# Kernel tuning notes

Measured on AMD Instinct MI355X. Metric: run time of the kernel, lower is better.

The kernel has to match this reference:

```python
import jax, jax.numpy as jnp
import numpy as np

B, N, K, H = 8, 1024, 16, 4
EMB = 1024

def lrelu(x):
    return jnp.where(x >= 0, x, 0.2 * x)

def bn(x, g, b):
    # eval-mode BatchNorm with running_mean=0, running_var=1
    inv = 1.0 / np.sqrt(1.0 + 1e-5)
    shape = (1, -1) + (1,) * (x.ndim - 2)
    return x * (g * inv).reshape(shape) + b.reshape(shape)

def conv1x1(x, w):
    # 1x1 conv == channel matmul; x: (B,C,...), w: (O,C)
    return jnp.einsum('bc...,oc->bo...', x, w)

def knn_idx(x, k):
    # x: (B,C,N); negative squared pairwise distance, top-k largest = nearest
    inner = -2.0 * jnp.einsum('bcn,bcm->bnm', x, x)
    xx = jnp.sum(x * x, axis=1)                      # (B,N)
    pd = -xx[:, :, None] - inner - xx[:, None, :]
    return jax.lax.top_k(pd, k)[1]                   # (B,N,k)

def graph_feature(x, idx):
    b = x.shape[0]
    xt = jnp.transpose(x, (0, 2, 1))                 # (B,N,C)
    nbr = xt[jnp.arange(b)[:, None, None], idx]      # (B,N,K,C) gather
    ctr = jnp.broadcast_to(xt[:, :, None, :], nbr.shape)
    f = jnp.concatenate([nbr - ctr, ctr], axis=-1)   # (B,N,K,2C)
    return jnp.transpose(f, (0, 3, 1, 2))            # (B,2C,N,K)

def mak(x, y, w0, g0, b0, wm, gm, bm, w1, go, bo, ws, gs, bs, out_ch, in_ch):
    # Multi-head adaptive kernel: generate per-point (out,in,H) weights from y, apply to x
    Bc, _, Nc, Kc = x.shape
    y = lrelu(bn(conv1x1(y, w0), g0, b0))
    y = lrelu(bn(conv1x1(y, wm), gm, bm))
    y = conv1x1(y, w1)                               # (B, out*in*H, N, K)
    w = jnp.transpose(y, (0, 2, 3, 1)).reshape(Bc, Nc, Kc, out_ch, in_ch, H)
    xt = jnp.transpose(x, (0, 2, 3, 1))              # (B,N,K,in)
    # per-head matmul then sum over heads == single einsum over i and h
    out = jnp.einsum('bnkoih,bnki->bonk', w, xt)
    out = bn(out, go, bo)
    idt = bn(conv1x1(x, ws), gs, bs)                 # shortcut (in != out)
    return lrelu(out + idt)


def setup_inputs() -> dict:
    ks = jax.random.split(jax.random.key(0), 48)
    it = iter(range(48))
    def nrm(shape, fan):
        return jax.random.normal(ks[next(it)], shape, jnp.float32) / np.sqrt(fan)
    def gam(c):
        return jax.random.uniform(ks[next(it)], (c,), jnp.float32, 0.5, 1.5)
    def bet(c):
        return 0.1 * jax.random.normal(ks[next(it)], (c,), jnp.float32)
    d = {}
    d['x'] = jax.random.normal(ks[next(it)], (B, 3, N), jnp.float32)
    def mak_params(p, feat_c):
        d[p + '_w0'] = nrm((64, feat_c), feat_c); d[p + '_g0'] = gam(64); d[p + '_b0'] = bet(64)
        d[p + '_wm'] = nrm((64, 64), 64); d[p + '_gm'] = gam(64); d[p + '_bm'] = bet(64)
        d[p + '_w1'] = nrm((64 * 6 * H, 64), 64)
        d[p + '_go'] = gam(64); d[p + '_bo'] = bet(64)
        d[p + '_ws'] = nrm((64, 6), 6); d[p + '_gs'] = gam(64); d[p + '_bs'] = bet(64)
    mak_params('m1', 6)
    mak_params('m2', 128)
    d['w3'] = nrm((128, 128), 128); d['g3'] = gam(128); d['b3'] = bet(128)
    d['w4'] = nrm((256, 256), 256); d['g4'] = gam(256); d['b4'] = bet(256)
    d['w5'] = nrm((EMB, 512), 512); d['g5'] = gam(EMB); d['b5'] = bet(EMB)
    d['wl1'] = nrm((512, 2 * EMB), 2 * EMB); d['bn4_g'] = gam(512); d['bn4_b'] = bet(512)
    d['wl2'] = nrm((256, 512), 512); d['bl2'] = bet(256); d['bn5_g'] = gam(256); d['bn5_b'] = bet(256)
    d['wl3'] = nrm((49, 256), 256); d['bl3'] = bet(49)
    return d


def reference(x, m1_w0, m1_g0, m1_b0, m1_wm, m1_gm, m1_bm, m1_w1, m1_go, m1_bo, m1_ws, m1_gs, m1_bs, m2_w0, m2_g0, m2_b0, m2_wm, m2_gm, m2_bm, m2_w1, m2_go, m2_bo, m2_ws, m2_gs, m2_bs, w3, g3, b3, w4, g4, b4, w5, g5, b5, wl1, bn4_g, bn4_b, wl2, bl2, bn5_g, bn5_b, wl3, bl3):
    idx = knn_idx(x, K)                              # common_idx from points
    geo = graph_feature(x, idx)                      # (B,6,N,K); feat_x == geo_x at stage 1
    h = mak(geo, geo, m1_w0, m1_g0, m1_b0, m1_wm, m1_gm, m1_bm, m1_w1, m1_go, m1_bo, m1_ws, m1_gs, m1_bs, 64, 6)
    x1 = h.max(axis=-1)                              # (B,64,N)
    feat2 = graph_feature(x1, idx)                   # (B,128,N,K)
    h = mak(geo, feat2, m2_w0, m2_g0, m2_b0, m2_wm, m2_gm, m2_bm, m2_w1, m2_go, m2_bo, m2_ws, m2_gs, m2_bs, 64, 6)
    x2 = h.max(axis=-1)                              # (B,64,N)
    x3 = lrelu(bn(conv1x1(graph_feature(x2, idx), w3), g3, b3)).max(axis=-1)   # (B,128,N)
    x4 = lrelu(bn(conv1x1(graph_feature(x3, idx), w4), g4, b4)).max(axis=-1)   # (B,256,N)
    xc = jnp.concatenate([x1, x2, x3, x4], axis=1)   # (B,512,N)
    x5 = lrelu(bn(conv1x1(xc, w5), g5, b5))          # (B,EMB,N)
    xp = jnp.concatenate([x5.max(axis=-1), x5.mean(axis=-1)], axis=1)  # (B,2*EMB)
    xf = lrelu(bn(xp @ wl1.T, bn4_g, bn4_b))
    xf = lrelu(bn(xf @ wl2.T + bl2, bn5_g, bn5_b))
    return xf @ wl3.T + bl3                           # (B,49)
```

## Files before the change

kernel.cpp:

```cpp
#include <hip/hip_runtime.h>
#include <math.h>

#define BB 8
#define NN 1024
#define KK 16
#define NKP (NN*KK)
#define BN_INV 0.99999500003749981f

typedef unsigned short u16;
typedef __attribute__((ext_vector_type(8))) short short8;
typedef __attribute__((ext_vector_type(4))) float f32x4;

#define MFMA16(a,b,c) __builtin_amdgcn_mfma_f32_16x16x32_bf16(a,b,c,0,0,0)

__device__ __forceinline__ float lrelu(float v) { return v >= 0.f ? v : 0.2f * v; }

__device__ __forceinline__ u16 f2bf(float f) {
  union { float f; unsigned u; } v; v.f = f;
  unsigned r = v.u + 0x7fff + ((v.u >> 16) & 1);
  return (u16)(r >> 16);
}
__device__ __forceinline__ float bf2f(u16 s) {
  union { unsigned u; float f; } v; v.u = ((unsigned)s) << 16;
  return v.f;
}

constexpr size_t OFF_IDX   = 0;
constexpr size_t OFF_X1P   = 524288;
constexpr size_t OFF_X2P   = 1572864;
constexpr size_t OFF_X3P   = 2621440;
constexpr size_t OFF_MUV   = 2621440;
constexpr size_t OFF_X4P   = 4718592;
constexpr size_t OFF_GEO   = 4718592;
constexpr size_t OFF_PMAX  = 8912896;
constexpr size_t OFF_PSUM  = 9437184;
constexpr size_t OFF_XP    = 9961472;
constexpr size_t OFF_XF1   = 10027008;
constexpr size_t OFF_XF2   = 10043392;
constexpr size_t OFF_M1WM  = 10055680;
constexpr size_t OFF_M1W1S = 10063872;
constexpr size_t OFF_M2W0S = 10117120;
constexpr size_t OFF_M2WM  = 10133504;
constexpr size_t OFF_M2W1S = 10141696;
constexpr size_t OFF_W3S   = 10194944;
constexpr size_t OFF_W4S   = 10227712;
constexpr size_t OFF_W5    = 10358784;
constexpr size_t OFF_WL1T  = 11407360;
constexpr size_t OFF_WL2T  = 15601664;
constexpr size_t OFF_WL3T  = 16125952;
constexpr size_t OFF_UV3   = 16177152;
constexpr size_t OFF_EY0   = 16177152;
constexpr size_t OFF_UV4   = 20371456;

struct SSeg { const float* w; const float* g; u16* dst; int O; int C; int cpl2; int ch; int stk; int start; };
struct SArgs { SSeg seg[6]; int total; };

__global__ __launch_bounds__(256) void prep_scale_bf16(SArgs a) {
  const int tid = blockIdx.x * 256 + threadIdx.x;
  if (tid >= a.total) return;
  int s = 0;
  #pragma unroll
  for (int i = 1; i < 6; ++i) if (tid >= a.seg[i].start) s = i;
  const SSeg sg = a.seg[s];
  const int e = tid - sg.start;
  const int o2 = e >> sg.cpl2;
  const int c = e & ((1 << sg.cpl2) - 1);
  float v = 0.f;
  if (sg.stk) {
    const int half = sg.O >> 1;
    const int o = o2 & (half - 1);
    const int CIN = 2 * sg.C;
    const float wd = sg.w[o * CIN + c];
    v = (o2 < half) ? wd : (sg.w[o * CIN + sg.C + c] - wd);
    v *= sg.g[o] * BN_INV;
  } else if (c < sg.C) {
    v = sg.w[o2 * sg.C + c];
    if (sg.ch && c >= sg.ch) v -= sg.w[o2 * sg.C + c - sg.ch];
    v *= sg.g[o2] * BN_INV;
  }
  sg.dst[(size_t)(c >> 5) * (sg.O * 32) + o2 * 32 + (c & 31)] = f2bf(v);
}

__global__ __launch_bounds__(256) void prep_w1s_bf16(
    const float* __restrict__ w1a, const float* __restrict__ wsa,
    const float* __restrict__ goa, const float* __restrict__ gsa,
    const float* __restrict__ w1b, const float* __restrict__ wsb,
    const float* __restrict__ gob, const float* __restrict__ gsb,
    u16* __restrict__ dsta, u16* __restrict__ dstb) {
  const int tid = blockIdx.x * 256 + threadIdx.x;
  if (tid >= 64 * 416) return;
  const float* w1 = blockIdx.y ? w1b : w1a;
  const float* wsm = blockIdx.y ? wsb : wsa;
  const float* go = blockIdx.y ? gob : goa;
  const float* gs = blockIdx.y ? gsb : gsa;
  u16* dst = blockIdx.y ? dstb : dsta;
  const int o = tid / 416, ci = tid - o * 416;
  float v = 0.f;
  if (ci < 384) {
    const int ii = ci >> 6, ch = ci & 63;
    const int base = (o * 24 + ii * 4) * 64 + ch;
    v = go[o] * BN_INV * (w1[base] + w1[base + 64] + w1[base + 128] + w1[base + 192]);
  } else if (ci < 390) {
    v = gs[o] * BN_INV * wsm[o * 6 + (ci - 384)];
  }
  dst[(size_t)(ci >> 5) * 2048 + o * 32 + (ci & 31)] = f2bf(v);
}

struct TSeg { const float* w; const float* g; float* dst; int O; int C; int start; };
struct TArgs3 { TSeg seg[3]; int total; };

__global__ __launch_bounds__(256) void prep_transpose_f32(TArgs3 a) {
  const int tid = blockIdx.x * 256 + threadIdx.x;
  if (tid >= a.total) return;
  int s = 0;
  #pragma unroll
  for (int i = 1; i < 3; ++i) if (tid >= a.seg[i].start) s = i;
  const TSeg sg = a.seg[s];
  const int e = tid - sg.start;
  const int c = e / sg.O;
  const int o = e - c * sg.O;
  float v = sg.w[o * sg.C + c];
  if (sg.g) v *= sg.g[o] * BN_INV;
  sg.dst[e] = v;
}

__global__ __launch_bounds__(256) void knn_kernel(const float* __restrict__ x, int* __restrict__ idxout) {
  const int wid  = (blockIdx.x * blockDim.x + threadIdx.x) >> 6;
  const int lane = threadIdx.x & 63;
  const int b = wid >> 10;
  const int n = wid & (NN - 1);
  const float* xb = x + b * 3 * NN;
  const float x0n = xb[n], x1n = xb[NN + n], x2n = xb[2 * NN + n];
  const float xxn = x0n * x0n + x1n * x1n + x2n * x2n;
  float pd[16];
  #pragma unroll
  for (int j = 0; j < 16; ++j) {
    const int m = j * 64 + lane;
    const float x0 = xb[m], x1 = xb[NN + m], x2 = xb[2 * NN + m];
    const float dot = x0n * x0 + x1n * x1 + x2n * x2;
    const float xxm = x0 * x0 + x1 * x1 + x2 * x2;
    pd[j] = 2.f * dot - xxn - xxm;
  }
  for (int r = 0; r < 16; ++r) {
    float bv = pd[0]; int bj = 0;
    #pragma unroll
    for (int j = 1; j < 16; ++j) if (pd[j] > bv) { bv = pd[j]; bj = j; }
    int bm = bj * 64 + lane;
    #pragma unroll
    for (int off = 32; off > 0; off >>= 1) {
      const float ov = __shfl_down(bv, off);
      const int   om = __shfl_down(bm, off);
      if (ov > bv || (ov == bv && om < bm)) { bv = ov; bm = om; }
    }
    bm = __shfl(bm, 0);
    if (lane == 0) idxout[wid * KK + r] = bm;
    const int  cj   = bm >> 6;
    const bool mine = (bm & 63) == lane;
    #pragma unroll
    for (int j = 0; j < 16; ++j) if (mine && j == cj) pd[j] = -INFINITY;
  }
}

__device__ __forceinline__ short8 bfrag64(const u16* T, int pl, int quad, int c0) {
  const int pos = ((c0 >> 3) + quad) ^ (pl & 7);
  return *(const short8*)(T + pl * 64 + pos * 8);
}
__device__ __forceinline__ void writeD64(u16* T, int pl, int quad, const f32x4 a,
                                         const float* __restrict__ bias, int obase) {
  union { ushort4 v; u16 s[4]; } pk;
  #pragma unroll
  for (int r = 0; r < 4; ++r) pk.s[r] = f2bf(lrelu(a[r] + bias[obase + quad * 4 + r]));
  const int g = (obase + quad * 4) >> 3;
  const int pos = g ^ (pl & 7);
  *(ushort4*)(T + pl * 64 + pos * 8 + (quad & 1) * 4) = pk.v;
}

__global__ __launch_bounds__(256) void mak1_uv(
    const float* __restrict__ x, const float* __restrict__ w0,
    const float* __restrict__ g0, const float* __restrict__ b0,
    u16* __restrict__ MUV) {
  const int tid = blockIdx.x * 256 + threadIdx.x;
  if (tid >= BB * NN * 64) return;
  const int o = tid & 63;
  const int p = tid >> 6;
  const int b = p >> 10, n = p & (NN - 1);
  const float* xb = x + b * 3 * NN;
  const float gg = g0[o] * BN_INV;
  float u = 0.f, v = 0.f;
  #pragma unroll
  for (int i = 0; i < 3; ++i) {
    const float wd = w0[o * 6 + i];
    const float wc = w0[o * 6 + 3 + i];
    const float c = xb[i * NN + n];
    u += wd * c;
    v += (wc - wd) * c;
  }
  MUV[(size_t)p * 128 + o]      = f2bf(gg * u);
  MUV[(size_t)p * 128 + 64 + o] = f2bf(gg * v + b0[o]);
}

__global__ __launch_bounds__(256) void mak_edge_build(
    const float* __restrict__ x, const int* __restrict__ idxb,
    const u16* __restrict__ MUV, u16* __restrict__ EY0,
    u16* __restrict__ GEO, int writeGeo) {
  const int tid = blockIdx.x * 256 + threadIdx.x;
  const int cg = tid & 7;
  const int e = tid >> 3;
  const int b = e >> 14;
  const int nk = e & 16383;
  const int n = nk >> 4;
  const int nbr = idxb[e] & (NN - 1);
  union { uint4 q; u16 s[8]; } uu, vv, rr;
  uu.q = *(const uint4*)(MUV + (size_t)(b * NN + nbr) * 128 + cg * 8);
  vv.q = *(const uint4*)(MUV + (size_t)(b * NN + n) * 128 + 64 + cg * 8);
  #pragma unroll
  for (int j = 0; j < 8; ++j) rr.s[j] = f2bf(lrelu(bf2f(uu.s[j]) + bf2f(vv.s[j])));
  *(uint4*)(EY0 + (size_t)e * 64 + cg * 8) = rr.q;
  if (writeGeo && cg == 0) {
    const float* xb = x + b * 3 * NN;
    union { uint4 q; u16 s[8]; } g;
    #pragma unroll
    for (int i = 0; i < 3; ++i) {
      const float fc = xb[i * NN + n];
      g.s[i]     = f2bf(xb[i * NN + nbr] - fc);
      g.s[3 + i] = f2bf(fc);
    }
    g.s[6] = 0; g.s[7] = 0;
    *(uint4*)(GEO + (size_t)e * 8) = g.q;
  }
}

__global__ __launch_bounds__(256) void mak23_mfma(
    const u16* __restrict__ EY0, const u16* __restrict__ GEO,
    const u16* __restrict__ wmb, const float* __restrict__ bmv,
    const u16* __restrict__ w1s, const float* __restrict__ bov, const float* __restrict__ bsv,
    u16* __restrict__ Xoutp) {
  __shared__ __align__(16) u16 YMs[64 * 64];

  const int t = threadIdx.x;
  const int b = blockIdx.z;
  const int w = t >> 6, l = t & 63;
  const int quad = l >> 4, l15 = l & 15;
  const int pl = w * 16 + l15;
  const int cq8 = quad * 8;
  const int nvtx = blockIdx.x * 4 + w;
  const size_t eL = ((size_t)(b * NN + nvtx)) * 16 + l15;

  union { short8 v; u16 s[8]; } gq;
  gq.v = *(const short8*)(GEO + eL * 8);
  float ge[6];
  #pragma unroll
  for (int ii = 0; ii < 6; ++ii) ge[ii] = bf2f(gq.s[ii]);
  const short8 bgv = (quad == 0) ? gq.v : (short8)(short)0;

  f32x4 acc[4];
  #pragma unroll
  for (int i = 0; i < 4; ++i) acc[i] = (f32x4)0.f;
  #pragma unroll
  for (int kc = 0; kc < 2; ++kc) {
    const short8 bf = *(const short8*)(EY0 + eL * 64 + kc * 32 + cq8);
    #pragma unroll
    for (int at = 0; at < 4; ++at) {
      const short8 af = *(const short8*)(wmb + (size_t)(kc * 64 + at * 16 + l15) * 32 + cq8);
      acc[at] = MFMA16(af, bf, acc[at]);
    }
  }
  #pragma unroll
  for (int at = 0; at < 4; ++at) writeD64(YMs, pl, quad, acc[at], bmv, at * 16);

  short8 bf3[2];
  #pragma unroll
  for (int kc = 0; kc < 2; ++kc) bf3[kc] = bfrag64(YMs, pl, quad, kc * 32);

  #pragma unroll
  for (int i = 0; i < 4; ++i) acc[i] = (f32x4)0.f;
  #pragma unroll
  for (int ii = 0; ii < 6; ++ii) {
    f32x4 tacc[4];
    #pragma unroll
    for (int i = 0; i < 4; ++i) tacc[i] = (f32x4)0.f;
    #pragma unroll
    for (int kc = 0; kc < 2; ++kc) {
      #pragma unroll
      for (int at = 0; at < 4; ++at) {
        const short8 af = *(const short8*)(w1s + (size_t)((ii * 2 + kc) * 64 + at * 16 + l15) * 32 + cq8);
        tacc[at] = MFMA16(af, bf3[kc], tacc[at]);
      }
    }
    const float g = ge[ii];
    #pragma unroll
    for (int at = 0; at < 4; ++at) acc[at] += g * tacc[at];
  }
  #pragma unroll
  for (int at = 0; at < 4; ++at) {
    const short8 af = *(const short8*)(w1s + (size_t)(12 * 64 + at * 16 + l15) * 32 + cq8);
    acc[at] = MFMA16(af, bgv, acc[at]);
  }

  u16* orow = Xoutp + (size_t)(b * NN + nvtx) * 64;
  #pragma unroll
  for (int at = 0; at < 4; ++at) {
    union { ushort4 v; u16 s[4]; } pk;
    #pragma unroll
    for (int r = 0; r < 4; ++r) {
      const int o = at * 16 + quad * 4 + r;
      float v = lrelu(acc[at][r] + bov[o] + bsv[o]);
      v = fmaxf(v, __shfl_xor(v, 1));
      v = fmaxf(v, __shfl_xor(v, 2));
      v = fmaxf(v, __shfl_xor(v, 4));
      v = fmaxf(v, __shfl_xor(v, 8));
      pk.s[r] = f2bf(v);
    }
    if (l15 == 0) *(ushort4*)(orow + at * 16 + quad * 4) = pk.v;
  }
}

template<int CH, int COUT2>
__global__ __launch_bounds__(256) void dense_uv(
    const u16* __restrict__ srcp, const u16* __restrict__ w2,
    const float* __restrict__ bias, u16* __restrict__ UV) {
  constexpr int COUT = COUT2 / 2;
  constexpr int NCH = CH / 32;
  const int t = threadIdx.x;
  const int b = blockIdx.z;
  const int w = t >> 6, l = t & 63;
  const int quad = l >> 4, l15 = l & 15;
  const int cq8 = quad * 8;
  int n0, ow0;
  if constexpr (COUT2 >= 256) { n0 = blockIdx.x * 64; ow0 = blockIdx.y * 256 + w * 64; }
  else { n0 = blockIdx.x * 128 + (w >> 1) * 64; ow0 = (w & 1) * 64; }

  f32x4 acc[4][4];
  #pragma unroll
  for (int i = 0; i < 4; ++i)
    #pragma unroll
    for (int j = 0; j < 4; ++j) acc[i][j] = (f32x4)0.f;

  #pragma unroll
  for (int k = 0; k < NCH; ++k) {
    short8 bfr[4];
    #pragma unroll
    for (int pg = 0; pg < 4; ++pg) {
      const int n = n0 + pg * 16 + l15;
      bfr[pg] = *(const short8*)(srcp + (size_t)(b * NN + n) * CH + k * 32 + cq8);
    }
    #pragma unroll
    for (int at = 0; at < 4; ++at) {
      const short8 af = *(const short8*)(w2 + ((size_t)(k * COUT2 + ow0 + at * 16 + l15)) * 32 + cq8);
      #pragma unroll
      for (int pg = 0; pg < 4; ++pg) acc[at][pg] = MFMA16(af, bfr[pg], acc[at][pg]);
    }
  }

  #pragma unroll
  for (int at = 0; at < 4; ++at) {
    const int o0 = ow0 + at * 16 + quad * 4;
    const bool isv = (o0 >= COUT);
    float bb[4];
    #pragma unroll
    for (int r = 0; r < 4; ++r) bb[r] = isv ? bias[o0 + r - COUT] : 0.f;
    #pragma unroll
    for (int pg = 0; pg < 4; ++pg) {
      const int n = n0 + pg * 16 + l15;
      union { ushort4 v; u16 s[4]; } pk;
      #pragma unroll
      for (int r = 0; r < 4; ++r) pk.s[r] = f2bf(acc[at][pg][r] + bb[r]);
      *(ushort4*)(UV + (size_t)(b * NN + n) * COUT2 + o0) = pk.v;
    }
  }
}

__device__ __forceinline__ float4 ubf4(ushort4 q) {
  float4 f;
  f.x = bf2f(q.x); f.y = bf2f(q.y); f.z = bf2f(q.z); f.w = bf2f(q.w);
  return f;
}

template<int COUT>
__global__ __launch_bounds__(256) void gather_max(
    const u16* __restrict__ UV, const int* __restrict__ idxb,
    u16* __restrict__ Xoutp) {
  constexpr int CG = COUT / 4;
  const int tid = blockIdx.x * 256 + threadIdx.x;
  const int cg = tid & (CG - 1);
  const int P = tid / CG;
  const int b = P >> 10;
  const int n = P & (NN - 1);

  const float4 vv = ubf4(*(const ushort4*)(UV + (size_t)P * (2 * COUT) + COUT + 4 * cg));
  const int4* ip = (const int4*)(idxb + (size_t)b * NKP + n * 16);
  float4 m = {-INFINITY, -INFINITY, -INFINITY, -INFINITY};
  #pragma unroll
  for (int kq = 0; kq < 4; ++kq) {
    const int4 iv = ip[kq];
    const int mr[4] = { iv.x & (NN - 1), iv.y & (NN - 1), iv.z & (NN - 1), iv.w & (NN - 1) };
    ushort4 uq[4];
    #pragma unroll
    for (int j = 0; j < 4; ++j)
      uq[j] = *(const ushort4*)(UV + (size_t)(b * NN + mr[j]) * (2 * COUT) + 4 * cg);
    #pragma unroll
    for (int j = 0; j < 4; ++j) {
      const float4 uu = ubf4(uq[j]);
      float4 s;
      s.x = uu.x + vv.x; s.y = uu.y + vv.y; s.z = uu.z + vv.z; s.w = uu.w + vv.w;
      m.x = fmaxf(m.x, fmaxf(s.x, 0.2f * s.x));
      m.y = fmaxf(m.y, fmaxf(s.y, 0.2f * s.y));
      m.z = fmaxf(m.z, fmaxf(s.z, 0.2f * s.z));
      m.w = fmaxf(m.w, fmaxf(s.w, 0.2f * s.w));
    }
  }
  union { ushort4 v; u16 s[4]; } pk;
  pk.s[0] = f2bf(m.x); pk.s[1] = f2bf(m.y); pk.s[2] = f2bf(m.z); pk.s[3] = f2bf(m.w);
  *(ushort4*)(Xoutp + (size_t)P * COUT + 4 * cg) = pk.v;
}

__global__ __launch_bounds__(256) void conv5_mfma(
    const u16* __restrict__ X1P, const u16* __restrict__ X2P,
    const u16* __restrict__ X3P, const u16* __restrict__ X4P,
    const u16* __restrict__ w5b, const float* __restrict__ b5,
    float* __restrict__ PMAX, float* __restrict__ PSUM) {
  const int t = threadIdx.x;
  const int b = blockIdx.z;
  const int n0 = blockIdx.x * 64;
  const int w = t >> 6, l = t & 63;
  const int quad = l >> 4, l15 = l & 15;
  const int cq8 = quad * 8;
  const int ow0 = blockIdx.y * 256 + w * 64;

  f32x4 acc[4][4];
  #pragma unroll
  for (int i = 0; i < 4; ++i)
    #pragma unroll
    for (int j = 0; j < 4; ++j) acc[i][j] = (f32x4)0.f;

  #pragma unroll 4
  for (int k = 0; k < 16; ++k) {
    const int c = k * 32 + cq8;
    short8 bfr[4];
    #pragma unroll
    for (int pg = 0; pg < 4; ++pg) {
      const int n = n0 + pg * 16 + l15;
      const u16* src; int cc;
      if (c < 64)       { src = X1P + (size_t)(b * NN + n) * 64;  cc = c; }
      else if (c < 128) { src = X2P + (size_t)(b * NN + n) * 64;  cc = c - 64; }
      else if (c < 256) { src = X3P + (size_t)(b * NN + n) * 128; cc = c - 128; }
      else              { src = X4P + (size_t)(b * NN + n) * 256; cc = c - 256; }
      bfr[pg] = *(const short8*)(src + cc);
    }
    #pragma unroll
    for (int at = 0; at < 4; ++at) {
      const short8 af = *(const short8*)(w5b + ((size_t)(k * 1024 + ow0 + at * 16 + l15)) * 32 + cq8);
      #pragma unroll
      for (int pg = 0; pg < 4; ++pg) acc[at][pg] = MFMA16(af, bfr[pg], acc[at][pg]);
    }
  }

  #pragma unroll
  for (int at = 0; at < 4; ++at) {
    f32x4 pmx, psm;
    #pragma unroll
    for (int r = 0; r < 4; ++r) {
      const float bb = b5[ow0 + at * 16 + quad * 4 + r];
      float m = -INFINITY, s = 0.f;
      #pragma unroll
      for (int pg = 0; pg < 4; ++pg) {
        const float v = lrelu(acc[at][pg][r] + bb);
        m = fmaxf(m, v); s += v;
      }
      #pragma unroll
      for (int msk = 1; msk < 16; msk <<= 1) {
        m = fmaxf(m, __shfl_xor(m, msk));
        s += __shfl_xor(s, msk);
      }
      pmx[r] = m; psm[r] = s;
    }
    if (l15 == 0) {
      float* dm = PMAX + (size_t)(b * 16 + blockIdx.x) * 1024 + ow0 + at * 16 + quad * 4;
      float* ds = PSUM + (size_t)(b * 16 + blockIdx.x) * 1024 + ow0 + at * 16 + quad * 4;
      *(f32x4*)dm = pmx;
      *(f32x4*)ds = psm;
    }
  }
}

__global__ __launch_bounds__(256) void reduce5(const float* __restrict__ PMAX, const float* __restrict__ PSUM,
                                               float* __restrict__ XPg) {
  const int tid = blockIdx.x * 256 + threadIdx.x;
  const int b = tid >> 10, o = tid & 1023;
  float m = -INFINITY, s = 0.f;
  for (int pt = 0; pt < 16; ++pt) {
    m = fmaxf(m, PMAX[(size_t)(b * 16 + pt) * 1024 + o]);
    s += PSUM[(size_t)(b * 16 + pt) * 1024 + o];
  }
  XPg[b * 2048 + o] = m;
  XPg[b * 2048 + 1024 + o] = s * (1.f / 1024.f);
}

__global__ __launch_bounds__(256) void fc1_kernel(const float* __restrict__ XPg, const float* __restrict__ wl1t,
                                                  const float* __restrict__ bn4_b, float* __restrict__ XF1) {
  __shared__ float red[64 * 5];
  const int t = threadIdx.x;
  const int b = blockIdx.y;
  const int o = blockIdx.x * 64 + (t & 63);
  const int cq = t >> 6;
  const float* xp = XPg + b * 2048;
  float acc = 0.f;
  for (int c = cq * 512; c < cq * 512 + 512; ++c) acc = fmaf(wl1t[c * 512 + o], xp[c], acc);
  red[(t & 63) * 5 + cq] = acc;
  __syncthreads();
  if (t < 64) {
    const int oo = blockIdx.x * 64 + t;
    const float v = red[t * 5] + red[t * 5 + 1] + red[t * 5 + 2] + red[t * 5 + 3] + bn4_b[oo];
    XF1[b * 512 + oo] = lrelu(v);
  }
}

__global__ __launch_bounds__(256) void fc2_kernel(const float* __restrict__ XF1, const float* __restrict__ wl2t,
                                                  const float* __restrict__ bl2, const float* __restrict__ bn5_g,
                                                  const float* __restrict__ bn5_b, float* __restrict__ XF2) {
  __shared__ float red[64 * 5];
  const int t = threadIdx.x;
  const int b = blockIdx.y;
  const int o = blockIdx.x * 64 + (t & 63);
  const int cq = t >> 6;
  const float* xf = XF1 + b * 512;
  float acc = 0.f;
  for (int c = cq * 128; c < cq * 128 + 128; ++c) acc = fmaf(wl2t[c * 256 + o], xf[c], acc);
  red[(t & 63) * 5 + cq] = acc;
  __syncthreads();
  if (t < 64) {
    const int oo = blockIdx.x * 64 + t;
    const float bias = bl2[oo] * (bn5_g[oo] * BN_INV) + bn5_b[oo];
    const float v = red[t * 5] + red[t * 5 + 1] + red[t * 5 + 2] + red[t * 5 + 3] + bias;
    XF2[b * 256 + oo] = lrelu(v);
  }
}

__global__ __launch_bounds__(256) void fc3_kernel(const float* __restrict__ XF2, const float* __restrict__ wl3t,
                                                  const float* __restrict__ bl3, float* __restrict__ out) {
  __shared__ float red[64 * 5];
  const int t = threadIdx.x;
  const int b = blockIdx.y;
  const int ol = t & 63;
  const int cq = t >> 6;
  const float* xf = XF2 + b * 256;
  float acc = 0.f;
  if (ol < 49) for (int c = cq * 64; c < cq * 64 + 64; ++c) acc = fmaf(wl3t[c * 49 + ol], xf[c], acc);
  red[ol * 5 + cq] = acc;
  __syncthreads();
  if (t < 49) out[b * 49 + t] = red[t * 5] + red[t * 5 + 1] + red[t * 5 + 2] + red[t * 5 + 3] + bl3[t];
}

extern "C" void kernel_launch(void* const* d_in, const int* in_sizes, int n_in,
                              void* d_out, int out_size, void* d_ws, size_t ws_size,
                              hipStream_t stream) {
  (void)in_sizes; (void)n_in; (void)out_size; (void)ws_size;
  const float* x     = (const float*)d_in[0];
  const float* m1_w0 = (const float*)d_in[1];
  const float* m1_g0 = (const float*)d_in[2];
  const float* m1_b0 = (const float*)d_in[3];
  const float* m1_wm = (const float*)d_in[4];
  const float* m1_gm = (const float*)d_in[5];
  const float* m1_bm = (const float*)d_in[6];
  const float* m1_w1 = (const float*)d_in[7];
  const float* m1_go = (const float*)d_in[8];
  const float* m1_bo = (const float*)d_in[9];
  const float* m1_ws = (const float*)d_in[10];
  const float* m1_gs = (const float*)d_in[11];
  const float* m1_bs = (const float*)d_in[12];
  const float* m2_w0 = (const float*)d_in[13];
  const float* m2_g0 = (const float*)d_in[14];
  const float* m2_b0 = (const float*)d_in[15];
  const float* m2_wm = (const float*)d_in[16];
  const float* m2_gm = (const float*)d_in[17];
  const float* m2_bm = (const float*)d_in[18];
  const float* m2_w1 = (const float*)d_in[19];
  const float* m2_go = (const float*)d_in[20];
  const float* m2_bo = (const float*)d_in[21];
  const float* m2_ws = (const float*)d_in[22];
  const float* m2_gs = (const float*)d_in[23];
  const float* m2_bs = (const float*)d_in[24];
  const float* w3    = (const float*)d_in[25];
  const float* g3    = (const float*)d_in[26];
  const float* b3    = (const float*)d_in[27];
  const float* w4    = (const float*)d_in[28];
  const float* g4    = (const float*)d_in[29];
  const float* b4    = (const float*)d_in[30];
  const float* w5    = (const float*)d_in[31];
  const float* g5    = (const float*)d_in[32];
  const float* b5    = (const float*)d_in[33];
  const float* wl1   = (const float*)d_in[34];
  const float* bn4_g = (const float*)d_in[35];
  const float* bn4_b = (const float*)d_in[36];
  const float* wl2   = (const float*)d_in[37];
  const float* bl2   = (const float*)d_in[38];
  const float* bn5_g = (const float*)d_in[39];
  const float* bn5_b = (const float*)d_in[40];
  const float* wl3   = (const float*)d_in[41];
  const float* bl3   = (const float*)d_in[42];

  char* wsb = (char*)d_ws;
  int*  IDX  = (int*)(wsb + OFF_IDX);
  u16*  X1P  = (u16*)(wsb + OFF_X1P);
  u16*  X2P  = (u16*)(wsb + OFF_X2P);
  u16*  X3P  = (u16*)(wsb + OFF_X3P);
  u16*  X4P  = (u16*)(wsb + OFF_X4P);
  u16*  MUV  = (u16*)(wsb + OFF_MUV);
  u16*  GEO  = (u16*)(wsb + OFF_GEO);
  u16*  EY0  = (u16*)(wsb + OFF_EY0);
  float* PMAX = (float*)(wsb + OFF_PMAX);
  float* PSUM = (float*)(wsb + OFF_PSUM);
  float* XPg  = (float*)(wsb + OFF_XP);
  float* XF1  = (float*)(wsb + OFF_XF1);
  float* XF2  = (float*)(wsb + OFF_XF2);
  u16*  M1WM = (u16*)(wsb + OFF_M1WM);
  u16*  M1W1S = (u16*)(wsb + OFF_M1W1S);
  u16*  M2W0S = (u16*)(wsb + OFF_M2W0S);
  u16*  M2WM = (u16*)(wsb + OFF_M2WM);
  u16*  M2W1S = (u16*)(wsb + OFF_M2W1S);
  u16*  W3S  = (u16*)(wsb + OFF_W3S);
  u16*  W4S  = (u16*)(wsb + OFF_W4S);
  u16*  W5B  = (u16*)(wsb + OFF_W5);
  float* WL1T = (float*)(wsb + OFF_WL1T);
  float* WL2T = (float*)(wsb + OFF_WL2T);
  float* WL3T = (float*)(wsb + OFF_WL3T);
  u16*  UV3  = (u16*)(wsb + OFF_UV3);
  u16*  UV4  = (u16*)(wsb + OFF_UV4);

  SArgs sa; int st = 0;
  auto sset = [&](int i, const float* w, const float* g, u16* dst, int O, int C, int cpl2, int ch, int stk) {
    sa.seg[i].w = w; sa.seg[i].g = g; sa.seg[i].dst = dst; sa.seg[i].O = O; sa.seg[i].C = C;
    sa.seg[i].cpl2 = cpl2; sa.seg[i].ch = ch; sa.seg[i].stk = stk; sa.seg[i].start = st;
    st += O << cpl2;
  };
  sset(0, m1_wm, m1_gm, M1WM, 64, 64, 6, 0, 0);
  sset(1, m2_w0, m2_g0, M2W0S, 128, 64, 6, 0, 1);
  sset(2, m2_wm, m2_gm, M2WM, 64, 64, 6, 0, 0);
  sset(3, w3, g3, W3S, 256, 64, 6, 0, 1);
  sset(4, w4, g4, W4S, 512, 128, 7, 0, 1);
  sset(5, w5, g5, W5B, 1024, 512, 9, 0, 0);
  sa.total = st;

  TArgs3 ta; int tt = 0;
  auto tset = [&](int i, const float* w, const float* g, float* dst, int O, int C) {
    ta.seg[i].w = w; ta.seg[i].g = g; ta.seg[i].dst = dst; ta.seg[i].O = O; ta.seg[i].C = C;
    ta.seg[i].start = tt; tt += O * C;
  };
  tset(0, wl1, bn4_g, WL1T, 512, 2048);
  tset(1, wl2, bn5_g, WL2T, 256, 512);
  tset(2, wl3, nullptr, WL3T, 49, 256);
  ta.total = tt;

  hipLaunchKernelGGL(prep_scale_bf16, dim3((sa.total + 255) / 256), dim3(256), 0, stream, sa);
  hipLaunchKernelGGL(prep_w1s_bf16, dim3(104, 2), dim3(256), 0, stream,
                     m1_w1, m1_ws, m1_go, m1_gs, m2_w1, m2_ws, m2_go, m2_gs, M1W1S, M2W1S);
  hipLaunchKernelGGL(prep_transpose_f32, dim3((ta.total + 255) / 256), dim3(256), 0, stream, ta);

  hipLaunchKernelGGL(knn_kernel, dim3(2048), dim3(256), 0, stream, x, IDX);

  hipLaunchKernelGGL(mak1_uv, dim3((BB * NN * 64 + 255) / 256), dim3(256), 0, stream,
                     x, m1_w0, m1_g0, m1_b0, MUV);
  hipLaunchKernelGGL(mak_edge_build, dim3(4096), dim3(256), 0, stream, x, IDX, MUV, EY0, GEO, 1);
  hipLaunchKernelGGL(mak23_mfma, dim3(256, 1, BB), dim3(256), 0, stream,
                     EY0, GEO, M1WM, m1_bm, M1W1S, m1_bo, m1_bs, X1P);

  hipLaunchKernelGGL((dense_uv<64, 128>), dim3(8, 1, BB), dim3(256), 0, stream, X1P, M2W0S, m2_b0, MUV);
  hipLaunchKernelGGL(mak_edge_build, dim3(4096), dim3(256), 0, stream, x, IDX, MUV, EY0, GEO, 0);
  hipLaunchKernelGGL(mak23_mfma, dim3(256, 1, BB), dim3(256), 0, stream,
                     EY0, GEO, M2WM, m2_bm, M2W1S, m2_bo, m2_bs, X2P);

  hipLaunchKernelGGL((dense_uv<64, 256>), dim3(16, 1, BB), dim3(256), 0, stream, X2P, W3S, b3, UV3);
  hipLaunchKernelGGL((gather_max<128>), dim3(1024), dim3(256), 0, stream, UV3, IDX, X3P);
  hipLaunchKernelGGL((dense_uv<128, 512>), dim3(16, 2, BB), dim3(256), 0, stream, X3P, W4S, b4, UV4);
  hipLaunchKernelGGL((gather_max<256>), dim3(2048), dim3(256), 0, stream, UV4, IDX, X4P);

  hipLaunchKernelGGL(conv5_mfma, dim3(16, 4, BB), dim3(256), 0, stream,
                     X1P, X2P, X3P, X4P, W5B, b5, PMAX, PSUM);
  hipLaunchKernelGGL(reduce5, dim3(32), dim3(256), 0, stream, PMAX, PSUM, XPg);

  hipLaunchKernelGGL(fc1_kernel, dim3(8, BB), dim3(256), 0, stream, XPg, WL1T, bn4_b, XF1);
  hipLaunchKernelGGL(fc2_kernel, dim3(4, BB), dim3(256), 0, stream, XF1, WL2T, bl2, bn5_g, bn5_b, XF2);
  hipLaunchKernelGGL(fc3_kernel, dim3(1, BB), dim3(256), 0, stream, XF2, WL3T, bl3, (float*)d_out);
}
```

Before: 409.0 us.

## Process four points per wave in mak23 to reuse weight fragments

Each wave in mak23_mfma now handles four vertices instead of one, so every weight A-fragment loaded from w1s and wmb feeds four MFMAs instead of one. Shared memory gets a separate 64x64 staging tile per wave, and the grid shrinks fourfold to match. This cuts redundant global and L2 weight loads. In exchange it raises register pressure (4x4 accumulators plus temporaries) and leaves fewer blocks in flight, which launch_bounds(256,2) tries to keep in check.

Result: faster. 384.3 us (-6.0%).

```diff
diff --git a/kernel.cpp b/kernel.cpp
--- a/kernel.cpp
+++ b/kernel.cpp
@@ -230,88 +230,113 @@
   }
 }
 
-__global__ __launch_bounds__(256) void mak23_mfma(
+__global__ __launch_bounds__(256, 2) void mak23_mfma(
     const u16* __restrict__ EY0, const u16* __restrict__ GEO,
     const u16* __restrict__ wmb, const float* __restrict__ bmv,
     const u16* __restrict__ w1s, const float* __restrict__ bov, const float* __restrict__ bsv,
     u16* __restrict__ Xoutp) {
-  __shared__ __align__(16) u16 YMs[64 * 64];
+  __shared__ __align__(16) u16 YMs[4][64 * 64];
 
   const int t = threadIdx.x;
   const int b = blockIdx.z;
   const int w = t >> 6, l = t & 63;
   const int quad = l >> 4, l15 = l & 15;
-  const int pl = w * 16 + l15;
   const int cq8 = quad * 8;
-  const int nvtx = blockIdx.x * 4 + w;
-  const size_t eL = ((size_t)(b * NN + nvtx)) * 16 + l15;
-
-  union { short8 v; u16 s[8]; } gq;
-  gq.v = *(const short8*)(GEO + eL * 8);
-  float ge[6];
-  #pragma unroll
-  for (int ii = 0; ii < 6; ++ii) ge[ii] = bf2f(gq.s[ii]);
-  const short8 bgv = (quad == 0) ? gq.v : (short8)(short)0;
-
-  f32x4 acc[4];
-  #pragma unroll
-  for (int i = 0; i < 4; ++i) acc[i] = (f32x4)0.f;
-  #pragma unroll
-  for (int kc = 0; kc < 2; ++kc) {
-    const short8 bf = *(const short8*)(EY0 + eL * 64 + kc * 32 + cq8);
-    #pragma unroll
-    for (int at = 0; at < 4; ++at) {
-      const short8 af = *(const short8*)(wmb + (size_t)(kc * 64 + at * 16 + l15) * 32 + cq8);
-      acc[at] = MFMA16(af, bf, acc[at]);
-    }
-  }
-  #pragma unroll
-  for (int at = 0; at < 4; ++at) writeD64(YMs, pl, quad, acc[at], bmv, at * 16);
-
-  short8 bf3[2];
-  #pragma unroll
-  for (int kc = 0; kc < 2; ++kc) bf3[kc] = bfrag64(YMs, pl, quad, kc * 32);
-
-  #pragma unroll
-  for (int i = 0; i < 4; ++i) acc[i] = (f32x4)0.f;
+  const int p0 = blockIdx.x * 16 + w * 4;
+  u16* myYM = YMs[w];
+
+  float ge[4][6];
+  short8 bgv[4];
+  size_t eL[4];
+  #pragma unroll
+  for (int pg = 0; pg < 4; ++pg) {
+    eL[pg] = ((size_t)(b * NN + p0 + pg)) * 16 + l15;
+    union { short8 v; u16 s[8]; } gq;
+    gq.v = *(const short8*)(GEO + eL[pg] * 8);
+    #pragma unroll
+    for (int ii = 0; ii < 6; ++ii) ge[pg][ii] = bf2f(gq.s[ii]);
+    bgv[pg] = (quad == 0) ? gq.v : (short8)(short)0;
+  }
+
+  #pragma unroll
+  for (int pg = 0; pg < 4; ++pg) {
+    f32x4 a2[4];
+    #pragma unroll
+    for (int i = 0; i < 4; ++i) a2[i] = (f32x4)0.f;
+    #pragma unroll
+    for (int kc = 0; kc < 2; ++kc) {
+      const short8 bf = *(const short8*)(EY0 + eL[pg] * 64 + kc * 32 + cq8);
+      #pragma unroll
+      for (int at = 0; at < 4; ++at) {
+        const short8 af = *(const short8*)(wmb + (size_t)(kc * 64 + at * 16 + l15) * 32 + cq8);
+        a2[at] = MFMA16(af, bf, a2[at]);
+      }
+    }
+    #pragma unroll
+    for (int at = 0; at < 4; ++at) writeD64(myYM, pg * 16 + l15, quad, a2[at], bmv, at * 16);
+  }
+
+  short8 bf3[4][2];
+  #pragma unroll
+  for (int pg = 0; pg < 4; ++pg)
+    #pragma unroll
+    for (int kc = 0; kc < 2; ++kc)
+      bf3[pg][kc] = bfrag64(myYM, pg * 16 + l15, quad, kc * 32);
+
+  f32x4 acc[4][4];
+  #pragma unroll
+  for (int pg = 0; pg < 4; ++pg)
+    #pragma unroll
+    for (int at = 0; at < 4; ++at) acc[pg][at] = (f32x4)0.f;
+
   #pragma unroll
   for (int ii = 0; ii < 6; ++ii) {
-    f32x4 tacc[4];
-    #pragma unroll
-    for (int i = 0; i < 4; ++i) tacc[i] = (f32x4)0.f;
+    f32x4 tac[4][4];
+    #pragma unroll
+    for (int pg = 0; pg < 4; ++pg)
+      #pragma unroll
+      for (int at = 0; at < 4; ++at) tac[pg][at] = (f32x4)0.f;
     #pragma unroll
     for (int kc = 0; kc < 2; ++kc) {
       #pragma unroll
       for (int at = 0; at < 4; ++at) {
         const short8 af = *(const short8*)(w1s + (size_t)((ii * 2 + kc) * 64 + at * 16 + l15) * 32 + cq8);
-        tacc[at] = MFMA16(af, bf3[kc], tacc[at]);
+        #pragma unroll
+        for (int pg = 0; pg < 4; ++pg) tac[pg][at] = MFMA16(af, bf3[pg][kc], tac[pg][at]);
       }
     }
-    const float g = ge[ii];
-    #pragma unroll
-    for (int at = 0; at < 4; ++at) acc[at] += g * tacc[at];
+    #pragma unroll
+    for (int pg = 0; pg < 4; ++pg) {
+      const float g = ge[pg][ii];
+      #pragma unroll
+      for (int at = 0; at < 4; ++at) acc[pg][at] += g * tac[pg][at];
+    }
   }
   #pragma unroll
   for (int at = 0; at < 4; ++at) {
     const short8 af = *(const short8*)(w1s + (size_t)(12 * 64 + at * 16 + l15) * 32 + cq8);
-    acc[at] = MFMA16(af, bgv, acc[at]);
-  }
-
-  u16* orow = Xoutp + (size_t)(b * NN + nvtx) * 64;
-  #pragma unroll
-  for (int at = 0; at < 4; ++at) {
-    union { ushort4 v; u16 s[4]; } pk;
-    #pragma unroll
-    for (int r = 0; r < 4; ++r) {
-      const int o = at * 16 + quad * 4 + r;
-      float v = lrelu(acc[at][r] + bov[o] + bsv[o]);
-      v = fmaxf(v, __shfl_xor(v, 1));
-      v = fmaxf(v, __shfl_xor(v, 2));
-      v = fmaxf(v, __shfl_xor(v, 4));
-      v = fmaxf(v, __shfl_xor(v, 8));
-      pk.s[r] = f2bf(v);
-    }
-    if (l15 == 0) *(ushort4*)(orow + at * 16 + quad * 4) = pk.v;
+    #pragma unroll
+    for (int pg = 0; pg < 4; ++pg) acc[pg][at] = MFMA16(af, bgv[pg], acc[pg][at]);
+  }
+
+  #pragma unroll
+  for (int pg = 0; pg < 4; ++pg) {
+    u16* orow = Xoutp + (size_t)(b * NN + p0 + pg) * 64;
+    #pragma unroll
+    for (int at = 0; at < 4; ++at) {
+      union { ushort4 v; u16 s[4]; } pk;
+      #pragma unroll
+      for (int r = 0; r < 4; ++r) {
+        const int o = at * 16 + quad * 4 + r;
+        float v = lrelu(acc[pg][at][r] + bov[o] + bsv[o]);
+        v = fmaxf(v, __shfl_xor(v, 1));
+        v = fmaxf(v, __shfl_xor(v, 2));
+        v = fmaxf(v, __shfl_xor(v, 4));
+        v = fmaxf(v, __shfl_xor(v, 8));
+        pk.s[r] = f2bf(v);
+      }
+      if (l15 == 0) *(ushort4*)(orow + at * 16 + quad * 4) = pk.v;
+    }
   }
 }
 
@@ -661,12 +686,12 @@
   hipLaunchKernelGGL(mak1_uv, dim3((BB * NN * 64 + 255) / 256), dim3(256), 0, stream,
                      x, m1_w0, m1_g0, m1_b0, MUV);
   hipLaunchKernelGGL(mak_edge_build, dim3(4096), dim3(256), 0, stream, x, IDX, MUV, EY0, GEO, 1);
-  hipLaunchKernelGGL(mak23_mfma, dim3(256, 1, BB), dim3(256), 0, stream,
+  hipLaunchKernelGGL(mak23_mfma, dim3(64, 1, BB), dim3(256), 0, stream,
                      EY0, GEO, M1WM, m1_bm, M1W1S, m1_bo, m1_bs, X1P);
 
   hipLaunchKernelGGL((dense_uv<64, 128>), dim3(8, 1, BB), dim3(256), 0, stream, X1P, M2W0S, m2_b0, MUV);
   hipLaunchKernelGGL(mak_edge_build, dim3(4096), dim3(256), 0, stream, x, IDX, MUV, EY0, GEO, 0);
-  hipLaunchKernelGGL(mak23_mfma, dim3(256, 1, BB), dim3(256), 0, stream,
+  hipLaunchKernelGGL(mak23_mfma, dim3(64, 1, BB), dim3(256), 0, stream,
                      EY0, GEO, M2WM, m2_bm, M2W1S, m2_bo, m2_bs, X2P);
 
   hipLaunchKernelGGL((dense_uv<64, 256>), dim3(16, 1, BB), dim3(256), 0, stream, X2P, W3S, b3, UV3);
```
